# Performance work log

Hardware: AMD Instinct MI355X
Metric: run time of the kernel (lower is better)

## Reference

```python
import jax, jax.numpy as jnp
import numpy as np
from jax import lax

N, P, Z, L = 1000, 50000, 10, 5


def setup_inputs() -> dict:
    key = jax.random.key(0)
    ks = jax.random.split(key, 9)
    data = jax.random.normal(ks[0], (N, P), dtype=jnp.float32)
    mean_z = jax.random.normal(ks[1], (N, Z), dtype=jnp.float32)
    A = jax.random.normal(ks[2], (Z, Z), dtype=jnp.float32) * 0.1
    var_z = A @ A.T + 0.01 * jnp.eye(Z, dtype=jnp.float32)  # PSD
    mean_w = jax.random.normal(ks[3], (L, Z, P), dtype=jnp.float32) * 0.01
    var_w = jax.random.uniform(ks[4], (L, Z), dtype=jnp.float32) + 0.1   # positive
    alpha = jax.nn.softmax(jax.random.normal(ks[5], (L, Z, P), dtype=jnp.float32), axis=-1)
    tau_0 = jax.random.uniform(ks[6], (L, Z), dtype=jnp.float32) + 0.5   # positive prior precision
    pi = jax.nn.softmax(jax.random.normal(ks[7], (Z, P), dtype=jnp.float32), axis=-1)
    tau = jnp.array(1.0, dtype=jnp.float32)
    return dict(data=data, mean_z=mean_z, var_z=var_z, mean_w=mean_w,
                var_w=var_w, alpha=alpha, tau_0=tau_0, pi=pi, tau=tau)


def _log_bf(z, s2, s0):
    s0_inv = 1.0 / s0
    s2ps0inv = s2 + s0_inv
    return 0.5 * (jnp.log(s2) - jnp.log(s2ps0inv) + z ** 2 * (s0_inv / s2ps0inv))


def reference(data, mean_z, var_z, mean_w, var_w, alpha, tau_0, pi, tau):
    n_dim = data.shape[0]
    l_dim, z_dim, p_dim = mean_w.shape

    # FactorModel.moments
    mean_zz = mean_z.T @ mean_z + n_dim * var_z            # [z, z]
    # LoadingModel.moments (only mean_w moment is needed)
    W0 = jnp.sum(mean_w * alpha, axis=0)                    # [z, p]

    def factor_body(kdx, carry):
        W, mw, vw, al = carry
        not_k = jnp.where(jnp.arange(z_dim) != kdx, size=z_dim - 1)[0]  # [z-1]
        E_zpzk = mean_zz[kdx][not_k]                        # [z-1]
        E_zzk = mean_zz[kdx, kdx]                           # scalar
        Wk = W[kdx]                                         # [p]
        Wnk = W[not_k]                                      # [z-1, p]
        RtZk = mean_z[:, kdx] @ data - Wnk.T @ E_zpzk       # [p]

        def effect_body(ldx, ecarry):
            Wk, mw, vw, al = ecarry
            Wkl = Wk - mw[ldx, kdx] * al[ldx, kdx]          # [p] residualized
            E_RtZk = RtZk - E_zzk * Wkl                     # [p]
            u_var = jnp.reciprocal(tau * E_zzk + tau_0[ldx, kdx])  # scalar
            u_mean = tau * u_var * E_RtZk                   # [p]
            Z_s = E_RtZk / E_zzk * jnp.sqrt(E_zzk * tau)    # [p]
            s2_s = 1.0 / (E_zzk * tau)
            log_bf = _log_bf(Z_s, s2_s, tau_0[ldx, kdx])
            alpha_kl = jax.nn.softmax(jnp.log(pi[kdx]) + log_bf)   # [p]
            Wk_new = Wkl + u_mean * alpha_kl
            return (Wk_new,
                    mw.at[ldx, kdx].set(u_mean),
                    vw.at[ldx, kdx].set(u_var),
                    al.at[ldx, kdx].set(alpha_kl))

        Wk, mw, vw, al = lax.fori_loop(0, l_dim, effect_body, (Wk, mw, vw, al))
        return (W.at[kdx].set(Wk), mw, vw, al)

    W, mw, vw, al = lax.fori_loop(0, z_dim, factor_body, (W0, mean_w, var_w, alpha))
    return mw, vw, al
```

## Files before the change

kernel.cpp:

```cpp
#include <hip/hip_runtime.h>
#include <math.h>

#define N_DIM 1000
#define P_DIM 50000
#define Z_DIM 10
#define L_DIM 5
#define NSTEP 50

#define NTP 256
#define NBP 196
#define NSPLIT 4
#define NCHUNK 250

#define NT1 256
#define PPT 8
#define PBLK (NT1 * PPT)
#define NBLK 25
#define NWAVES (NBLK * 4)
#define SLOT_STRIDE 128
#define NEG_BIG (-3.0e38f)
#define SPIN_MAX 32768

constexpr size_t ZP       = (size_t)Z_DIM * P_DIM;
constexpr size_t OFF_PART = 0;
constexpr size_t PART_F   = (size_t)NSTEP * SLOT_STRIDE * 2;
constexpr size_t OFF_ZTRP = PART_F;
constexpr size_t OFF_W    = OFF_ZTRP + (size_t)NSPLIT * ZP;
constexpr size_t OFF_ZZ   = OFF_W + ZP;

constexpr size_t OUT_MW = 0;
constexpr size_t OUT_VW = (size_t)L_DIM * Z_DIM * P_DIM;
constexpr size_t OUT_AL = OUT_VW + (size_t)L_DIM * Z_DIM;

__global__ __launch_bounds__(NTP) void precompute_big(const float* __restrict__ data,
                                                      const float* __restrict__ mean_z,
                                                      const float* __restrict__ var_z,
                                                      const float* __restrict__ mw0,
                                                      const float* __restrict__ al0,
                                                      float* __restrict__ ws) {
    if (blockIdx.y == NSPLIT) {
        int bx = blockIdx.x;
        if (bx < Z_DIM * Z_DIM) {
            float* zz = ws + OFF_ZZ;
            int i = bx / Z_DIM, j = bx % Z_DIM;
            float s = 0.f;
            for (int n = threadIdx.x; n < N_DIM; n += NTP)
                s += mean_z[n * Z_DIM + i] * mean_z[n * Z_DIM + j];
            #pragma unroll
            for (int off = 32; off > 0; off >>= 1) s += __shfl_xor(s, off);
            __shared__ float ls[4];
            if ((threadIdx.x & 63) == 0) ls[threadIdx.x >> 6] = s;
            __syncthreads();
            if (threadIdx.x == 0) {
                float t = ls[0] + ls[1] + ls[2] + ls[3];
                zz[bx] = t + (float)N_DIM * var_z[bx];
            }
        } else {
            unsigned long long* part = reinterpret_cast<unsigned long long*>(ws + OFF_PART);
            int idx = (bx - Z_DIM * Z_DIM) * NTP + threadIdx.x;
            if (idx < NSTEP * SLOT_STRIDE) part[idx] = 0ULL;
        }
        return;
    }

    float* ZtRp = ws + OFF_ZTRP + (size_t)blockIdx.y * ZP;
    float* W    = ws + OFF_W;
    __shared__ float mzs[NCHUNK * Z_DIM];
    int n0 = blockIdx.y * NCHUNK;
    for (int i = threadIdx.x; i < NCHUNK * Z_DIM; i += NTP)
        mzs[i] = mean_z[n0 * Z_DIM + i];
    __syncthreads();
    int p = blockIdx.x * NTP + threadIdx.x;
    if (p >= P_DIM) return;

    float acc[Z_DIM];
    #pragma unroll
    for (int z = 0; z < Z_DIM; z++) acc[z] = 0.f;
    for (int r = 0; r < NCHUNK; r++) {
        float d = data[(size_t)(n0 + r) * P_DIM + p];
        #pragma unroll
        for (int z = 0; z < Z_DIM; z++) acc[z] = fmaf(mzs[r * Z_DIM + z], d, acc[z]);
    }
    #pragma unroll
    for (int z = 0; z < Z_DIM; z++) ZtRp[(size_t)z * P_DIM + p] = acc[z];

    if (blockIdx.y == 0) {
        #pragma unroll
        for (int z = 0; z < Z_DIM; z++) {
            float w = 0.f;
            #pragma unroll
            for (int l = 0; l < L_DIM; l++) {
                size_t io = ((size_t)l * Z_DIM + z) * P_DIM + p;
                w = fmaf(mw0[io], al0[io], w);
            }
            W[(size_t)z * P_DIM + p] = w;
        }
    }
}

__global__ __launch_bounds__(NT1) void steps_fused(const float* __restrict__ mw0,
                                                   const float* __restrict__ al0,
                                                   const float* __restrict__ pi,
                                                   const float* __restrict__ tau0,
                                                   const float* __restrict__ taup,
                                                   float* __restrict__ ws,
                                                   float* __restrict__ out) {
    const float* ZtRp = ws + OFF_ZTRP;
    const float* Wg   = ws + OFF_W;
    const float* zz   = ws + OFF_ZZ;
    unsigned long long* part = reinterpret_cast<unsigned long long*>(ws + OFF_PART);
    float* out_mw = out + OUT_MW;
    float* out_vw = out + OUT_VW;
    float* out_al = out + OUT_AL;

    __shared__ float bro[2][2];

    const int tid  = threadIdx.x;
    const int bid  = blockIdx.x;
    const int lane = tid & 63;
    const int wid  = tid >> 6;
    const int gw   = bid * 4 + wid;
    const int p0   = bid * PBLK + tid * PPT;
    const bool valid = p0 < P_DIM;
    const float tau = taup[0];
    const unsigned long long READY0 =
        ((unsigned long long)1u << 32) | (unsigned long long)__float_as_uint(NEG_BIG);

    float W[Z_DIM][PPT];
    #pragma unroll
    for (int z = 0; z < Z_DIM; z++)
        #pragma unroll
        for (int i = 0; i < PPT; i++) W[z][i] = 0.f;
    float mw_c[PPT], al_c[PPT], lpi[PPT], zk[PPT];
    #pragma unroll
    for (int i = 0; i < PPT; i++) { mw_c[i] = 0.f; al_c[i] = 0.f; lpi[i] = 0.f; zk[i] = 0.f; }
    if (valid) {
        #pragma unroll
        for (int z = 0; z < Z_DIM; z++) {
            float4 a = *reinterpret_cast<const float4*>(Wg + (size_t)z * P_DIM + p0);
            float4 b = *reinterpret_cast<const float4*>(Wg + (size_t)z * P_DIM + p0 + 4);
            W[z][0] = a.x; W[z][1] = a.y; W[z][2] = a.z; W[z][3] = a.w;
            W[z][4] = b.x; W[z][5] = b.y; W[z][6] = b.z; W[z][7] = b.w;
        }
        float4 ma = *reinterpret_cast<const float4*>(mw0 + p0);
        float4 mb = *reinterpret_cast<const float4*>(mw0 + p0 + 4);
        float4 aa = *reinterpret_cast<const float4*>(al0 + p0);
        float4 ab = *reinterpret_cast<const float4*>(al0 + p0 + 4);
        mw_c[0]=ma.x; mw_c[1]=ma.y; mw_c[2]=ma.z; mw_c[3]=ma.w;
        mw_c[4]=mb.x; mw_c[5]=mb.y; mw_c[6]=mb.z; mw_c[7]=mb.w;
        al_c[0]=aa.x; al_c[1]=aa.y; al_c[2]=aa.z; al_c[3]=aa.w;
        al_c[4]=ab.x; al_c[5]=ab.y; al_c[6]=ab.z; al_c[7]=ab.w;
        #pragma unroll
        for (int i = 0; i < PPT; i++) lpi[i] = __logf(pi[p0 + i]);
        #pragma unroll
        for (int y = 0; y < NSPLIT; y++) {
            const float* src = ZtRp + ((size_t)y * Z_DIM + 0) * P_DIM + p0;
            float4 a = *reinterpret_cast<const float4*>(src);
            float4 b = *reinterpret_cast<const float4*>(src + 4);
            zk[0]+=a.x; zk[1]+=a.y; zk[2]+=a.z; zk[3]+=a.w;
            zk[4]+=b.x; zk[5]+=b.y; zk[6]+=b.z; zk[7]+=b.w;
        }
    }

    float wk[PPT], r[PPT];
    #pragma unroll
    for (int i = 0; i < PPT; i++) { wk[i] = 0.f; r[i] = 0.f; }
    int k = 0, l = 0;

    #pragma unroll 1
    for (int s = 0; s < NSTEP; s++) {
        const float Ezz   = zz[k * Z_DIM + k];
        const float t0v   = tau0[l * Z_DIM + k];
        const float u_var = 1.f / (tau * Ezz + t0v);
        const float s2    = 1.f / (Ezz * tau);
        const float s0inv = 1.f / t0v;
        const float cq    = 0.5f * (tau / Ezz) * (s0inv / (s2 + s0inv));

        if (l == 0) {
            #pragma unroll
            for (int i = 0; i < PPT; i++) r[i] = zk[i];
            #pragma unroll
            for (int j = 0; j < Z_DIM; j++) {
                float c = (j == k) ? 0.f : zz[k * Z_DIM + j];
                #pragma unroll
                for (int i = 0; i < PPT; i++) r[i] = fmaf(-c, W[j][i], r[i]);
                if (j == k)
                    #pragma unroll
                    for (int i = 0; i < PPT; i++) wk[i] = W[j][i];
            }
        }

        float wkl[PPT], E[PPT], lgt[PPT];
        #pragma unroll
        for (int i = 0; i < PPT; i++) { wkl[i] = 0.f; E[i] = 0.f; lgt[i] = NEG_BIG; }
        if (valid) {
            #pragma unroll
            for (int i = 0; i < PPT; i++) {
                wkl[i] = wk[i] - mw_c[i] * al_c[i];
                E[i]   = fmaf(-Ezz, wkl[i], r[i]);
                lgt[i] = fmaf(cq * E[i], E[i], lpi[i]);
            }
        }
        float m4 = lgt[0];
        #pragma unroll
        for (int i = 1; i < PPT; i++) m4 = fmaxf(m4, lgt[i]);
        #pragma unroll
        for (int off = 32; off > 0; off >>= 1) m4 = fmaxf(m4, __shfl_xor(m4, off));
        const float Mw = m4;
        float esv[PPT];
        #pragma unroll
        for (int i = 0; i < PPT; i++) esv[i] = __expf(lgt[i] - Mw);
        float s4 = 0.f;
        #pragma unroll
        for (int i = 0; i < PPT; i++) s4 += esv[i];
        #pragma unroll
        for (int off = 32; off > 0; off >>= 1) s4 += __shfl_xor(s4, off);
        if (lane == 0) {
            unsigned long long v = ((unsigned long long)__float_as_uint(s4) << 32)
                                 | (unsigned long long)__float_as_uint(Mw);
            __hip_atomic_store(&part[(size_t)s * SLOT_STRIDE + gw], v, __ATOMIC_RELAXED,
                               __HIP_MEMORY_SCOPE_AGENT);
        }

        const size_t io = ((size_t)l * Z_DIM + k) * P_DIM + p0;
        float cc[PPT];
        #pragma unroll
        for (int i = 0; i < PPT; i++) cc[i] = 0.f;
        if (valid) {
            float um[PPT];
            #pragma unroll
            for (int i = 0; i < PPT; i++) um[i] = tau * u_var * E[i];
            *reinterpret_cast<float4*>(out_mw + io)     = make_float4(um[0],um[1],um[2],um[3]);
            *reinterpret_cast<float4*>(out_mw + io + 4) = make_float4(um[4],um[5],um[6],um[7]);
            #pragma unroll
            for (int i = 0; i < PPT; i++) cc[i] = um[i] * esv[i];
        }
        int kn = k, ln = l + 1;
        if (ln == L_DIM) { ln = 0; kn++; }
        float mw_n[PPT], al_n[PPT];
        #pragma unroll
        for (int i = 0; i < PPT; i++) { mw_n[i] = 0.f; al_n[i] = 0.f; }
        if (valid && s + 1 < NSTEP) {
            size_t ion = ((size_t)ln * Z_DIM + kn) * P_DIM + p0;
            float4 ma = *reinterpret_cast<const float4*>(mw0 + ion);
            float4 mb = *reinterpret_cast<const float4*>(mw0 + ion + 4);
            float4 aa = *reinterpret_cast<const float4*>(al0 + ion);
            float4 ab = *reinterpret_cast<const float4*>(al0 + ion + 4);
            mw_n[0]=ma.x; mw_n[1]=ma.y; mw_n[2]=ma.z; mw_n[3]=ma.w;
            mw_n[4]=mb.x; mw_n[5]=mb.y; mw_n[6]=mb.z; mw_n[7]=mb.w;
            al_n[0]=aa.x; al_n[1]=aa.y; al_n[2]=aa.z; al_n[3]=aa.w;
            al_n[4]=ab.x; al_n[5]=ab.y; al_n[6]=ab.z; al_n[7]=ab.w;
            if (ln == 0) {
                #pragma unroll
                for (int i = 0; i < PPT; i++) lpi[i] = __logf(pi[(size_t)kn * P_DIM + p0 + i]);
                #pragma unroll
                for (int i = 0; i < PPT; i++) zk[i] = 0.f;
                #pragma unroll
                for (int y = 0; y < NSPLIT; y++) {
                    const float* src = ZtRp + ((size_t)y * Z_DIM + kn) * P_DIM + p0;
                    float4 a = *reinterpret_cast<const float4*>(src);
                    float4 b = *reinterpret_cast<const float4*>(src + 4);
                    zk[0]+=a.x; zk[1]+=a.y; zk[2]+=a.z; zk[3]+=a.w;
                    zk[4]+=b.x; zk[5]+=b.y; zk[6]+=b.z; zk[7]+=b.w;
                }
            }
        }

        if (wid == 0) {
            const unsigned long long* sb = part + (size_t)s * SLOT_STRIDE;
            unsigned long long v0 = 0;
            unsigned long long v1 = (lane < NWAVES - 64) ? 0ULL : READY0;
            for (int it = 0; it < SPIN_MAX; it++) {
                if (!(unsigned)(v0 >> 32))
                    v0 = __hip_atomic_load(sb + lane,      __ATOMIC_RELAXED, __HIP_MEMORY_SCOPE_AGENT);
                if (!(unsigned)(v1 >> 32))
                    v1 = __hip_atomic_load(sb + 64 + lane, __ATOMIC_RELAXED, __HIP_MEMORY_SCOPE_AGENT);
                if ((unsigned)(v0 >> 32) && (unsigned)(v1 >> 32)) break;
            }
            float m0 = __uint_as_float((unsigned)v0), e0 = __uint_as_float((unsigned)(v0 >> 32));
            float m1 = __uint_as_float((unsigned)v1), e1 = __uint_as_float((unsigned)(v1 >> 32));
            float mm = fmaxf(m0, m1);
            #pragma unroll
            for (int off = 32; off > 0; off >>= 1) mm = fmaxf(mm, __shfl_xor(mm, off));
            float ss = e0 * __expf(m0 - mm) + e1 * __expf(m1 - mm);
            #pragma unroll
            for (int off = 32; off > 0; off >>= 1) ss += __shfl_xor(ss, off);
            if (lane == 0) { bro[s & 1][0] = mm; bro[s & 1][1] = ss; }
        }
        __syncthreads();
        const float M     = bro[s & 1][0];
        const float scale = __expf(Mw - M) / bro[s & 1][1];

        if (valid) {
            float a[PPT];
            #pragma unroll
            for (int i = 0; i < PPT; i++) {
                a[i]  = esv[i] * scale;
                wk[i] = fmaf(cc[i], scale, wkl[i]);
            }
            *reinterpret_cast<float4*>(out_al + io)     = make_float4(a[0],a[1],a[2],a[3]);
            *reinterpret_cast<float4*>(out_al + io + 4) = make_float4(a[4],a[5],a[6],a[7]);
        }
        if (tid == 0 && bid == 0) out_vw[l * Z_DIM + k] = u_var;

        if (l == L_DIM - 1) {
            #pragma unroll
            for (int j = 0; j < Z_DIM; j++)
                if (j == k)
                    #pragma unroll
                    for (int i = 0; i < PPT; i++) W[j][i] = wk[i];
        }
        #pragma unroll
        for (int i = 0; i < PPT; i++) { mw_c[i] = mw_n[i]; al_c[i] = al_n[i]; }
        k = kn; l = ln;
    }
}

extern "C" void kernel_launch(void* const* d_in, const int* in_sizes, int n_in,
                              void* d_out, int out_size, void* d_ws, size_t ws_size,
                              hipStream_t stream) {
    (void)in_sizes; (void)n_in; (void)out_size; (void)ws_size;
    const float* data   = (const float*)d_in[0];
    const float* mean_z = (const float*)d_in[1];
    const float* var_z  = (const float*)d_in[2];
    const float* mw0    = (const float*)d_in[3];
    const float* al0    = (const float*)d_in[5];
    const float* tau0   = (const float*)d_in[6];
    const float* pi     = (const float*)d_in[7];
    const float* taup   = (const float*)d_in[8];
    float* out = (float*)d_out;
    float* ws  = (float*)d_ws;

    precompute_big<<<dim3(NBP, NSPLIT + 1), NTP, 0, stream>>>(data, mean_z, var_z,
                                                              mw0, al0, ws);
    steps_fused<<<NBLK, NT1, 0, stream>>>(mw0, al0, pi, tau0, taup, ws, out);
}
```

Baseline: 468.7 us.

## Dedicate a poller wave per block and defer softmax normalization across steps

Adds a fifth wave per block whose only job is to spin on the global per-step partial (max, sum) slots, reduce them, and publish the result through an LDS slot. This removes the per-step __syncthreads and the wave-0 polling from the compute waves. The compute waves restructure the recurrence algebraically: they precompute E_base and h so the next step's logits need only the previous step's scale, which moves the grid-wide reduction off the critical path. Alpha writes and W updates are deferred by one step. The cost is extra registers, the launch_bounds(320,2) constraint, LDS spin loops, and more complex bookkeeping at factor boundaries.

```diff
diff --git a/kernel.cpp b/kernel.cpp
--- a/kernel.cpp
+++ b/kernel.cpp
@@ -12,14 +12,15 @@
 #define NSPLIT 4
 #define NCHUNK 250
 
-#define NT1 256
+#define NT1 320
 #define PPT 8
-#define PBLK (NT1 * PPT)
+#define PBLK 2048
 #define NBLK 25
-#define NWAVES (NBLK * 4)
+#define NPUB 100
 #define SLOT_STRIDE 128
 #define NEG_BIG (-3.0e38f)
-#define SPIN_MAX 32768
+#define SPIN_MAX 65536
+#define SPIN_MAX_LDS (1 << 20)
 
 constexpr size_t ZP       = (size_t)Z_DIM * P_DIM;
 constexpr size_t OFF_PART = 0;
@@ -98,13 +99,15 @@
     }
 }
 
-__global__ __launch_bounds__(NT1) void steps_fused(const float* __restrict__ mw0,
-                                                   const float* __restrict__ al0,
-                                                   const float* __restrict__ pi,
-                                                   const float* __restrict__ tau0,
-                                                   const float* __restrict__ taup,
-                                                   float* __restrict__ ws,
-                                                   float* __restrict__ out) {
+__device__ inline float4 ld4(const float* p) { return *reinterpret_cast<const float4*>(p); }
+
+__global__ __launch_bounds__(NT1, 2) void steps_fused(const float* __restrict__ mw0,
+                                                      const float* __restrict__ al0,
+                                                      const float* __restrict__ pi,
+                                                      const float* __restrict__ tau0,
+                                                      const float* __restrict__ taup,
+                                                      float* __restrict__ ws,
+                                                      float* __restrict__ out) {
     const float* ZtRp = ws + OFF_ZTRP;
     const float* Wg   = ws + OFF_W;
     const float* zz   = ws + OFF_ZZ;
@@ -113,93 +116,134 @@
     float* out_vw = out + OUT_VW;
     float* out_al = out + OUT_AL;
 
-    __shared__ float bro[2][2];
+    __shared__ unsigned long long lsl[NSTEP];
 
     const int tid  = threadIdx.x;
     const int bid  = blockIdx.x;
     const int lane = tid & 63;
     const int wid  = tid >> 6;
-    const int gw   = bid * 4 + wid;
-    const int p0   = bid * PBLK + tid * PPT;
+    const float tau = taup[0];
+
+    for (int i = tid; i < NSTEP; i += NT1) lsl[i] = 0ULL;
+    __syncthreads();
+
+    if (wid == 0) {
+        const unsigned long long READY0 =
+            ((unsigned long long)1u << 32) | (unsigned long long)__float_as_uint(NEG_BIG);
+        const bool has2 = lane < (NPUB - 64);
+        for (int s = 0; s < NSTEP; s++) {
+            const unsigned long long* sb = part + (size_t)s * SLOT_STRIDE;
+            unsigned long long v0 = 0, v1 = READY0;
+            for (int it = 0; it < SPIN_MAX; it++) {
+                v0 = __hip_atomic_load(sb + lane, __ATOMIC_RELAXED, __HIP_MEMORY_SCOPE_AGENT);
+                if (has2)
+                    v1 = __hip_atomic_load(sb + 64 + lane, __ATOMIC_RELAXED, __HIP_MEMORY_SCOPE_AGENT);
+                if ((unsigned)(v0 >> 32) && (unsigned)(v1 >> 32)) break;
+            }
+            float m0 = __uint_as_float((unsigned)v0), e0 = __uint_as_float((unsigned)(v0 >> 32));
+            float m1 = __uint_as_float((unsigned)v1), e1 = __uint_as_float((unsigned)(v1 >> 32));
+            float mm = fmaxf(m0, m1);
+            #pragma unroll
+            for (int off = 32; off > 0; off >>= 1) mm = fmaxf(mm, __shfl_xor(mm, off));
+            float ss = e0 * __expf(m0 - mm) + e1 * __expf(m1 - mm);
+            #pragma unroll
+            for (int off = 32; off > 0; off >>= 1) ss += __shfl_xor(ss, off);
+            if (lane == 0) {
+                unsigned long long v = ((unsigned long long)__float_as_uint(ss) << 32)
+                                     | (unsigned long long)__float_as_uint(mm);
+                __hip_atomic_store(&lsl[s], v, __ATOMIC_RELAXED, __HIP_MEMORY_SCOPE_WORKGROUP);
+                if (bid == 0) {
+                    int k = s / L_DIM, l = s % L_DIM;
+                    out_vw[l * Z_DIM + k] = 1.f / fmaf(tau, zz[k * Z_DIM + k], tau0[l * Z_DIM + k]);
+                }
+            }
+        }
+        return;
+    }
+
+    const int cw = wid - 1;
+    const int p0 = bid * PBLK + (cw * 64 + lane) * PPT;
     const bool valid = p0 < P_DIM;
-    const float tau = taup[0];
-    const unsigned long long READY0 =
-        ((unsigned long long)1u << 32) | (unsigned long long)__float_as_uint(NEG_BIG);
 
     float W[Z_DIM][PPT];
     #pragma unroll
     for (int z = 0; z < Z_DIM; z++)
         #pragma unroll
         for (int i = 0; i < PPT; i++) W[z][i] = 0.f;
-    float mw_c[PPT], al_c[PPT], lpi[PPT], zk[PPT];
-    #pragma unroll
-    for (int i = 0; i < PPT; i++) { mw_c[i] = 0.f; al_c[i] = 0.f; lpi[i] = 0.f; zk[i] = 0.f; }
+    float mw_c[PPT], al_c[PPT], lpi[PPT];
+    #pragma unroll
+    for (int i = 0; i < PPT; i++) { mw_c[i] = 0.f; al_c[i] = 0.f; lpi[i] = 0.f; }
+    float r[PPT], E_base[PPT], h[PPT];
+    #pragma unroll
+    for (int i = 0; i < PPT; i++) { r[i] = 0.f; E_base[i] = 0.f; h[i] = 0.f; }
+
     if (valid) {
         #pragma unroll
         for (int z = 0; z < Z_DIM; z++) {
-            float4 a = *reinterpret_cast<const float4*>(Wg + (size_t)z * P_DIM + p0);
-            float4 b = *reinterpret_cast<const float4*>(Wg + (size_t)z * P_DIM + p0 + 4);
-            W[z][0] = a.x; W[z][1] = a.y; W[z][2] = a.z; W[z][3] = a.w;
-            W[z][4] = b.x; W[z][5] = b.y; W[z][6] = b.z; W[z][7] = b.w;
-        }
-        float4 ma = *reinterpret_cast<const float4*>(mw0 + p0);
-        float4 mb = *reinterpret_cast<const float4*>(mw0 + p0 + 4);
-        float4 aa = *reinterpret_cast<const float4*>(al0 + p0);
-        float4 ab = *reinterpret_cast<const float4*>(al0 + p0 + 4);
+            float4 a = ld4(Wg + (size_t)z * P_DIM + p0);
+            float4 b = ld4(Wg + (size_t)z * P_DIM + p0 + 4);
+            W[z][0]=a.x; W[z][1]=a.y; W[z][2]=a.z; W[z][3]=a.w;
+            W[z][4]=b.x; W[z][5]=b.y; W[z][6]=b.z; W[z][7]=b.w;
+        }
+        float4 ma = ld4(mw0 + p0), mb = ld4(mw0 + p0 + 4);
+        float4 aa = ld4(al0 + p0), ab = ld4(al0 + p0 + 4);
         mw_c[0]=ma.x; mw_c[1]=ma.y; mw_c[2]=ma.z; mw_c[3]=ma.w;
         mw_c[4]=mb.x; mw_c[5]=mb.y; mw_c[6]=mb.z; mw_c[7]=mb.w;
         al_c[0]=aa.x; al_c[1]=aa.y; al_c[2]=aa.z; al_c[3]=aa.w;
         al_c[4]=ab.x; al_c[5]=ab.y; al_c[6]=ab.z; al_c[7]=ab.w;
-        #pragma unroll
-        for (int i = 0; i < PPT; i++) lpi[i] = __logf(pi[p0 + i]);
+        float4 pa = ld4(pi + p0), pb = ld4(pi + p0 + 4);
+        lpi[0]=__logf(pa.x); lpi[1]=__logf(pa.y); lpi[2]=__logf(pa.z); lpi[3]=__logf(pa.w);
+        lpi[4]=__logf(pb.x); lpi[5]=__logf(pb.y); lpi[6]=__logf(pb.z); lpi[7]=__logf(pb.w);
         #pragma unroll
         for (int y = 0; y < NSPLIT; y++) {
             const float* src = ZtRp + ((size_t)y * Z_DIM + 0) * P_DIM + p0;
-            float4 a = *reinterpret_cast<const float4*>(src);
-            float4 b = *reinterpret_cast<const float4*>(src + 4);
-            zk[0]+=a.x; zk[1]+=a.y; zk[2]+=a.z; zk[3]+=a.w;
-            zk[4]+=b.x; zk[5]+=b.y; zk[6]+=b.z; zk[7]+=b.w;
-        }
-    }
-
-    float wk[PPT], r[PPT];
-    #pragma unroll
-    for (int i = 0; i < PPT; i++) { wk[i] = 0.f; r[i] = 0.f; }
+            float4 a = ld4(src), b = ld4(src + 4);
+            r[0]+=a.x; r[1]+=a.y; r[2]+=a.z; r[3]+=a.w;
+            r[4]+=b.x; r[5]+=b.y; r[6]+=b.z; r[7]+=b.w;
+        }
+    }
+    #pragma unroll
+    for (int j = 1; j < Z_DIM; j++) {
+        float c = zz[j];
+        #pragma unroll
+        for (int i = 0; i < PPT; i++) r[i] = fmaf(-c, W[j][i], r[i]);
+    }
+    float Ezz = zz[0], t0v = tau0[0];
+    float tuv = tau / fmaf(tau, Ezz, t0v);
+    float s2 = 1.f / (Ezz * tau), s0i = 1.f / t0v;
+    float cq = 0.5f * (tau / Ezz) * (s0i / (s2 + s0i));
+    #pragma unroll
+    for (int i = 0; i < PPT; i++) {
+        float wklA = W[0][i] - mw_c[i] * al_c[i];
+        E_base[i] = fmaf(-Ezz, wklA, r[i]);
+    }
+
+    float wklP[PPT], ccP[PPT], esvP[PPT];
+    #pragma unroll
+    for (int i = 0; i < PPT; i++) { wklP[i] = 0.f; ccP[i] = 0.f; esvP[i] = 0.f; }
+    float MwP = 0.f, scale = 1.f;
+    int io_prev = 0;
     int k = 0, l = 0;
+    const int gw = bid * 4 + cw;
 
     #pragma unroll 1
     for (int s = 0; s < NSTEP; s++) {
-        const float Ezz   = zz[k * Z_DIM + k];
-        const float t0v   = tau0[l * Z_DIM + k];
-        const float u_var = 1.f / (tau * Ezz + t0v);
-        const float s2    = 1.f / (Ezz * tau);
-        const float s0inv = 1.f / t0v;
-        const float cq    = 0.5f * (tau / Ezz) * (s0inv / (s2 + s0inv));
-
-        if (l == 0) {
-            #pragma unroll
-            for (int i = 0; i < PPT; i++) r[i] = zk[i];
-            #pragma unroll
-            for (int j = 0; j < Z_DIM; j++) {
-                float c = (j == k) ? 0.f : zz[k * Z_DIM + j];
-                #pragma unroll
-                for (int i = 0; i < PPT; i++) r[i] = fmaf(-c, W[j][i], r[i]);
-                if (j == k)
-                    #pragma unroll
-                    for (int i = 0; i < PPT; i++) wk[i] = W[j][i];
-            }
-        }
-
-        float wkl[PPT], E[PPT], lgt[PPT];
-        #pragma unroll
-        for (int i = 0; i < PPT; i++) { wkl[i] = 0.f; E[i] = 0.f; lgt[i] = NEG_BIG; }
-        if (valid) {
-            #pragma unroll
-            for (int i = 0; i < PPT; i++) {
-                wkl[i] = wk[i] - mw_c[i] * al_c[i];
-                E[i]   = fmaf(-Ezz, wkl[i], r[i]);
-                lgt[i] = fmaf(cq * E[i], E[i], lpi[i]);
-            }
+        if (s > 0) {
+            unsigned long long v = 0;
+            for (int it = 0; it < SPIN_MAX_LDS; it++) {
+                v = __hip_atomic_load(&lsl[s - 1], __ATOMIC_RELAXED, __HIP_MEMORY_SCOPE_WORKGROUP);
+                if ((unsigned)(v >> 32)) break;
+            }
+            float M  = __uint_as_float((unsigned)v);
+            float ss = __uint_as_float((unsigned)(v >> 32));
+            scale = __expf(MwP - M) / ss;
+        }
+
+        float Ev[PPT], lgt[PPT], esv[PPT];
+        #pragma unroll
+        for (int i = 0; i < PPT; i++) {
+            Ev[i]  = fmaf(-h[i], scale, E_base[i]);
+            lgt[i] = valid ? fmaf(cq * Ev[i], Ev[i], lpi[i]) : NEG_BIG;
         }
         float m4 = lgt[0];
         #pragma unroll
@@ -207,12 +251,9 @@
         #pragma unroll
         for (int off = 32; off > 0; off >>= 1) m4 = fmaxf(m4, __shfl_xor(m4, off));
         const float Mw = m4;
-        float esv[PPT];
-        #pragma unroll
-        for (int i = 0; i < PPT; i++) esv[i] = __expf(lgt[i] - Mw);
         float s4 = 0.f;
         #pragma unroll
-        for (int i = 0; i < PPT; i++) s4 += esv[i];
+        for (int i = 0; i < PPT; i++) { esv[i] = __expf(lgt[i] - Mw); s4 += esv[i]; }
         #pragma unroll
         for (int off = 32; off > 0; off >>= 1) s4 += __shfl_xor(s4, off);
         if (lane == 0) {
@@ -222,97 +263,159 @@
                                __HIP_MEMORY_SCOPE_AGENT);
         }
 
-        const size_t io = ((size_t)l * Z_DIM + k) * P_DIM + p0;
-        float cc[PPT];
-        #pragma unroll
-        for (int i = 0; i < PPT; i++) cc[i] = 0.f;
-        if (valid) {
-            float um[PPT];
-            #pragma unroll
-            for (int i = 0; i < PPT; i++) um[i] = tau * u_var * E[i];
-            *reinterpret_cast<float4*>(out_mw + io)     = make_float4(um[0],um[1],um[2],um[3]);
-            *reinterpret_cast<float4*>(out_mw + io + 4) = make_float4(um[4],um[5],um[6],um[7]);
-            #pragma unroll
-            for (int i = 0; i < PPT; i++) cc[i] = um[i] * esv[i];
-        }
+        const int io_s = (l * Z_DIM + k) * P_DIM + p0;
         int kn = k, ln = l + 1;
         if (ln == L_DIM) { ln = 0; kn++; }
+        const bool more = (s + 1 < NSTEP);
+        const bool bnd  = more && (ln == 0);
+
         float mw_n[PPT], al_n[PPT];
         #pragma unroll
         for (int i = 0; i < PPT; i++) { mw_n[i] = 0.f; al_n[i] = 0.f; }
-        if (valid && s + 1 < NSTEP) {
+        float pin[PPT], zkn[PPT];
+        #pragma unroll
+        for (int i = 0; i < PPT; i++) { pin[i] = 1.f; zkn[i] = 0.f; }
+        if (valid && more) {
             size_t ion = ((size_t)ln * Z_DIM + kn) * P_DIM + p0;
-            float4 ma = *reinterpret_cast<const float4*>(mw0 + ion);
-            float4 mb = *reinterpret_cast<const float4*>(mw0 + ion + 4);
-            float4 aa = *reinterpret_cast<const float4*>(al0 + ion);
-            float4 ab = *reinterpret_cast<const float4*>(al0 + ion + 4);
+            float4 ma = ld4(mw0 + ion), mb = ld4(mw0 + ion + 4);
+            float4 aa = ld4(al0 + ion), ab = ld4(al0 + ion + 4);
             mw_n[0]=ma.x; mw_n[1]=ma.y; mw_n[2]=ma.z; mw_n[3]=ma.w;
             mw_n[4]=mb.x; mw_n[5]=mb.y; mw_n[6]=mb.z; mw_n[7]=mb.w;
             al_n[0]=aa.x; al_n[1]=aa.y; al_n[2]=aa.z; al_n[3]=aa.w;
             al_n[4]=ab.x; al_n[5]=ab.y; al_n[6]=ab.z; al_n[7]=ab.w;
-            if (ln == 0) {
-                #pragma unroll
-                for (int i = 0; i < PPT; i++) lpi[i] = __logf(pi[(size_t)kn * P_DIM + p0 + i]);
-                #pragma unroll
-                for (int i = 0; i < PPT; i++) zk[i] = 0.f;
+            if (bnd) {
+                float4 pa = ld4(pi + (size_t)kn * P_DIM + p0);
+                float4 pb = ld4(pi + (size_t)kn * P_DIM + p0 + 4);
+                pin[0]=pa.x; pin[1]=pa.y; pin[2]=pa.z; pin[3]=pa.w;
+                pin[4]=pb.x; pin[5]=pb.y; pin[6]=pb.z; pin[7]=pb.w;
                 #pragma unroll
                 for (int y = 0; y < NSPLIT; y++) {
                     const float* src = ZtRp + ((size_t)y * Z_DIM + kn) * P_DIM + p0;
-                    float4 a = *reinterpret_cast<const float4*>(src);
-                    float4 b = *reinterpret_cast<const float4*>(src + 4);
-                    zk[0]+=a.x; zk[1]+=a.y; zk[2]+=a.z; zk[3]+=a.w;
-                    zk[4]+=b.x; zk[5]+=b.y; zk[6]+=b.z; zk[7]+=b.w;
-                }
-            }
-        }
-
-        if (wid == 0) {
-            const unsigned long long* sb = part + (size_t)s * SLOT_STRIDE;
-            unsigned long long v0 = 0;
-            unsigned long long v1 = (lane < NWAVES - 64) ? 0ULL : READY0;
-            for (int it = 0; it < SPIN_MAX; it++) {
-                if (!(unsigned)(v0 >> 32))
-                    v0 = __hip_atomic_load(sb + lane,      __ATOMIC_RELAXED, __HIP_MEMORY_SCOPE_AGENT);
-                if (!(unsigned)(v1 >> 32))
-                    v1 = __hip_atomic_load(sb + 64 + lane, __ATOMIC_RELAXED, __HIP_MEMORY_SCOPE_AGENT);
-                if ((unsigned)(v0 >> 32) && (unsigned)(v1 >> 32)) break;
-            }
-            float m0 = __uint_as_float((unsigned)v0), e0 = __uint_as_float((unsigned)(v0 >> 32));
-            float m1 = __uint_as_float((unsigned)v1), e1 = __uint_as_float((unsigned)(v1 >> 32));
-            float mm = fmaxf(m0, m1);
-            #pragma unroll
-            for (int off = 32; off > 0; off >>= 1) mm = fmaxf(mm, __shfl_xor(mm, off));
-            float ss = e0 * __expf(m0 - mm) + e1 * __expf(m1 - mm);
-            #pragma unroll
-            for (int off = 32; off > 0; off >>= 1) ss += __shfl_xor(ss, off);
-            if (lane == 0) { bro[s & 1][0] = mm; bro[s & 1][1] = ss; }
-        }
-        __syncthreads();
-        const float M     = bro[s & 1][0];
-        const float scale = __expf(Mw - M) / bro[s & 1][1];
-
-        if (valid) {
+                    float4 a = ld4(src), b = ld4(src + 4);
+                    zkn[0]+=a.x; zkn[1]+=a.y; zkn[2]+=a.z; zkn[3]+=a.w;
+                    zkn[4]+=b.x; zkn[5]+=b.y; zkn[6]+=b.z; zkn[7]+=b.w;
+                }
+            }
+        }
+
+        if (valid && s > 0) {
             float a[PPT];
             #pragma unroll
-            for (int i = 0; i < PPT; i++) {
-                a[i]  = esv[i] * scale;
-                wk[i] = fmaf(cc[i], scale, wkl[i]);
-            }
-            *reinterpret_cast<float4*>(out_al + io)     = make_float4(a[0],a[1],a[2],a[3]);
-            *reinterpret_cast<float4*>(out_al + io + 4) = make_float4(a[4],a[5],a[6],a[7]);
-        }
-        if (tid == 0 && bid == 0) out_vw[l * Z_DIM + k] = u_var;
-
-        if (l == L_DIM - 1) {
+            for (int i = 0; i < PPT; i++) a[i] = esvP[i] * scale;
+            *reinterpret_cast<float4*>(out_al + io_prev)     = make_float4(a[0],a[1],a[2],a[3]);
+            *reinterpret_cast<float4*>(out_al + io_prev + 4) = make_float4(a[4],a[5],a[6],a[7]);
+        }
+
+        float wkl_s[PPT];
+        if (l == 0) {
+            if (s > 0) {
+                #pragma unroll
+                for (int j = 0; j < Z_DIM; j++)
+                    if (j == k - 1)
+                        #pragma unroll
+                        for (int i = 0; i < PPT; i++) W[j][i] = fmaf(ccP[i], scale, wklP[i]);
+                #pragma unroll
+                for (int i = 0; i < PPT; i++) r[i] = fmaf(-h[i], scale, r[i]);
+            }
+            float wkr[PPT];
+            #pragma unroll
+            for (int i = 0; i < PPT; i++) wkr[i] = 0.f;
             #pragma unroll
             for (int j = 0; j < Z_DIM; j++)
                 if (j == k)
                     #pragma unroll
-                    for (int i = 0; i < PPT; i++) W[j][i] = wk[i];
-        }
-        #pragma unroll
-        for (int i = 0; i < PPT; i++) { mw_c[i] = mw_n[i]; al_c[i] = al_n[i]; }
-        k = kn; l = ln;
+                    for (int i = 0; i < PPT; i++) wkr[i] = W[j][i];
+            #pragma unroll
+            for (int i = 0; i < PPT; i++) wkl_s[i] = wkr[i] - mw_c[i] * al_c[i];
+        } else {
+            #pragma unroll
+            for (int i = 0; i < PPT; i++)
+                wkl_s[i] = fmaf(ccP[i], scale, wklP[i]) - mw_c[i] * al_c[i];
+        }
+
+        float cc_s[PPT];
+        #pragma unroll
+        for (int i = 0; i < PPT; i++) cc_s[i] = 0.f;
+        if (valid) {
+            float um[PPT];
+            #pragma unroll
+            for (int i = 0; i < PPT; i++) um[i] = tuv * Ev[i];
+            *reinterpret_cast<float4*>(out_mw + io_s)     = make_float4(um[0],um[1],um[2],um[3]);
+            *reinterpret_cast<float4*>(out_mw + io_s + 4) = make_float4(um[4],um[5],um[6],um[7]);
+            #pragma unroll
+            for (int i = 0; i < PPT; i++) cc_s[i] = um[i] * esv[i];
+        }
+
+        if (more) {
+            float Ezz_n = zz[kn * Z_DIM + kn], t0v_n = tau0[ln * Z_DIM + kn];
+            float tuv_n = tau / fmaf(tau, Ezz_n, t0v_n);
+            float s2n = 1.f / (Ezz_n * tau), s0in = 1.f / t0v_n;
+            float cq_n = 0.5f * (tau / Ezz_n) * (s0in / (s2n + s0in));
+            if (!bnd) {
+                #pragma unroll
+                for (int i = 0; i < PPT; i++) {
+                    E_base[i] = fmaf(-Ezz_n, wkl_s[i] - mw_n[i] * al_n[i], r[i]);
+                    h[i]      = Ezz_n * cc_s[i];
+                }
+            } else {
+                float zkk = zz[kn * Z_DIM + k];
+                float rb[PPT];
+                #pragma unroll
+                for (int i = 0; i < PPT; i++) rb[i] = zkn[i];
+                #pragma unroll
+                for (int j = 0; j < Z_DIM; j++) {
+                    float c = (j == kn || j == k) ? 0.f : zz[kn * Z_DIM + j];
+                    #pragma unroll
+                    for (int i = 0; i < PPT; i++) rb[i] = fmaf(-c, W[j][i], rb[i]);
+                }
+                #pragma unroll
+                for (int i = 0; i < PPT; i++) {
+                    rb[i] = fmaf(-zkk, wkl_s[i], rb[i]);
+                    r[i]  = rb[i];
+                }
+                float wA[PPT];
+                #pragma unroll
+                for (int i = 0; i < PPT; i++) wA[i] = 0.f;
+                #pragma unroll
+                for (int j = 0; j < Z_DIM; j++)
+                    if (j == kn)
+                        #pragma unroll
+                        for (int i = 0; i < PPT; i++) wA[i] = W[j][i];
+                #pragma unroll
+                for (int i = 0; i < PPT; i++) {
+                    wA[i] -= mw_n[i] * al_n[i];
+                    E_base[i] = fmaf(-Ezz_n, wA[i], r[i]);
+                    h[i]      = zkk * cc_s[i];
+                    lpi[i]    = valid ? __logf(pin[i]) : 0.f;
+                }
+            }
+            cq = cq_n; tuv = tuv_n;
+        }
+
+        #pragma unroll
+        for (int i = 0; i < PPT; i++) {
+            esvP[i] = esv[i]; ccP[i] = cc_s[i]; wklP[i] = wkl_s[i];
+            mw_c[i] = mw_n[i]; al_c[i] = al_n[i];
+        }
+        MwP = Mw; io_prev = io_s; k = kn; l = ln;
+    }
+
+    {
+        unsigned long long v = 0;
+        for (int it = 0; it < SPIN_MAX_LDS; it++) {
+            v = __hip_atomic_load(&lsl[NSTEP - 1], __ATOMIC_RELAXED, __HIP_MEMORY_SCOPE_WORKGROUP);
+            if ((unsigned)(v >> 32)) break;
+        }
+        float M  = __uint_as_float((unsigned)v);
+        float ss = __uint_as_float((unsigned)(v >> 32));
+        float sc = __expf(MwP - M) / ss;
+        if (valid) {
+            float a[PPT];
+            #pragma unroll
+            for (int i = 0; i < PPT; i++) a[i] = esvP[i] * sc;
+            *reinterpret_cast<float4*>(out_al + io_prev)     = make_float4(a[0],a[1],a[2],a[3]);
+            *reinterpret_cast<float4*>(out_al + io_prev + 4) = make_float4(a[4],a[5],a[6],a[7]);
+        }
     }
 }
 
```

Measured after the change: 482.1 us. 2.8% more time.
